# Optimization experiments

Measured on AMD Instinct MI355X. Metric: run time of the kernel, lower is better.

## Reference

```python
import jax, jax.numpy as jnp
import numpy as np

B, CIN, H, W = 16, 128, 56, 56
COUT, KH, KW = 256, 3, 3
STRIDE = (1, 1)
PAD = ((1, 1), (1, 1))


def setup_inputs() -> dict:
    key = jax.random.key(0)
    k1, k2, k3 = jax.random.split(key, 3)
    x = jax.random.normal(k1, (B, CIN, H, W), dtype=jnp.float32)
    weight = jax.random.normal(k2, (COUT, CIN, KH, KW), dtype=jnp.float32) * 0.05
    bias = jax.random.normal(k3, (COUT,), dtype=jnp.float32)
    return {"x": x, "weight": weight, "bias": bias}


def reference(x, weight, bias):
    # Conv2d with zero padding, stride 1 -- identical math to the torch
    # unfold+expand+multiply+triple-sum path.
    dn = jax.lax.conv_dimension_numbers(x.shape, weight.shape, ("NCHW", "OIHW", "NCHW"))
    out = jax.lax.conv_general_dilated(x, weight, STRIDE, PAD, dimension_numbers=dn)
    out = out + bias[None, :, None, None]

    # Sparsity of the elementwise product patches * weight.
    # count_nonzero(x_patch * w) over all (b,hw,ww,co,ci,kh,kw) factorizes as
    # sum over windows of conv(1[x!=0], 1[w!=0]) -- same count without
    # materializing the [B,Hw,Ww,Co,Ci,kh,kw] tensor the torch code builds.
    co, ci, kh, kw = weight.shape
    hw, ww = out.shape[2], out.shape[3]
    num_elements = x.shape[0] * hw * ww * co * ci * kh * kw
    nz_map = jax.lax.conv_general_dilated(
        (x != 0).astype(jnp.float32),
        (weight != 0).astype(jnp.float32),
        STRIDE, PAD, dimension_numbers=dn)
    num_nonzero = jnp.sum(nz_map)
    layer_sparsity = (jnp.float32(num_elements) - num_nonzero) / jnp.float32(num_elements)
    return out, layer_sparsity
```

## Files before the change

### kernel.cpp

```cpp
#include <hip/hip_runtime.h>
#include <hip/hip_bf16.h>

typedef __attribute__((ext_vector_type(8))) short bf16x8;
typedef __attribute__((ext_vector_type(8))) unsigned short ushort8;
typedef __attribute__((ext_vector_type(4))) unsigned short ushort4v;
typedef __attribute__((ext_vector_type(4))) float f32x4;
typedef __attribute__((ext_vector_type(4))) unsigned int uint4v;

#define CIN_  128
#define BATCH 16
#define SP_   3136
#define CO_   256
#define NTOT  50176

#define XP_BYTES   13778944
#define WT_BYTES   589824
#define WS_NEEDED  14447104

__device__ __forceinline__ unsigned short f2bf(float f) {
    unsigned int u = __float_as_uint(f);
    u = (u + 0x7fffu + ((u >> 16) & 1u)) >> 16;
    return (unsigned short)u;
}

__device__ __forceinline__ void gl_lds16(const unsigned short* g, unsigned short* l) {
    __builtin_amdgcn_global_load_lds(
        (const __attribute__((address_space(1))) unsigned int*)g,
        (__attribute__((address_space(3))) unsigned int*)l, 16, 0, 0);
}

__global__ __launch_bounds__(256) void k_aux(
    const float* __restrict__ x, const float* __restrict__ w,
    unsigned short* __restrict__ Wt, unsigned short* __restrict__ xp,
    float* __restrict__ Wcnt, float* __restrict__ part)
{
    __shared__ float T[64][65];
    __shared__ float red9[4][9];
    const int blk = blockIdx.x;
    const int tid = threadIdx.x;

    if (blk < 288) {
        int base = (blk * 256 + tid) * 4;
        float4 v = *(const float4*)(w + base);
        #pragma unroll
        for (int j = 0; j < 4; ++j) {
            int e = base + j;
            int co = e / 1152;
            int r  = e - co * 1152;
            int ci = r / 9;
            int koff = r - ci * 9;
            Wt[(koff * 256 + co) * 128 + ci] = f2bf(((const float*)&v)[j]);
        }
    } else if (blk < 576) {
        int lane = tid & 63;
        int j = (blk - 288) * 4 + (tid >> 6);
        float c = 0.f;
        for (int co = lane; co < 256; co += 64)
            c += (w[(size_t)co * 1152 + j] != 0.0f) ? 1.f : 0.f;
        #pragma unroll
        for (int s = 32; s > 0; s >>= 1) c += __shfl_down(c, s, 64);
        if (lane == 0) Wcnt[j] = c;
    } else if (blk < 2624) {
        int bc = blk - 576;
        int ci = bc & 127;
        int b  = bc >> 7;
        const float* xpk = x + (size_t)bc * SP_;
        float cnt[9];
        #pragma unroll
        for (int k = 0; k < 9; ++k) cnt[k] = 0.f;
        for (int e = tid; e < SP_; e += 256) {
            float v = xpk[e];
            if (v != 0.f) {
                int h = e / 56, w_ = e - h * 56;
                float r0 = (h <= 54) ? 1.f : 0.f;
                float r2 = (h >= 1) ? 1.f : 0.f;
                float c0 = (w_ <= 54) ? 1.f : 0.f;
                float c2 = (w_ >= 1) ? 1.f : 0.f;
                cnt[0] += r0 * c0; cnt[1] += r0; cnt[2] += r0 * c2;
                cnt[3] += c0;      cnt[4] += 1.f; cnt[5] += c2;
                cnt[6] += r2 * c0; cnt[7] += r2; cnt[8] += r2 * c2;
            }
        }
        #pragma unroll
        for (int k = 0; k < 9; ++k) {
            #pragma unroll
            for (int s = 32; s > 0; s >>= 1) cnt[k] += __shfl_down(cnt[k], s, 64);
        }
        if ((tid & 63) == 0) {
            #pragma unroll
            for (int k = 0; k < 9; ++k) red9[tid >> 6][k] = cnt[k];
        }
        __syncthreads();
        if (tid < 9) {
            float s = red9[0][tid] + red9[1][tid] + red9[2][tid] + red9[3][tid];
            part[(ci * 9 + tid) * 16 + b] = s;
        }
    } else if (blk < 4192) {
        int i = blk - 2624;
        int sp0 = (i % 49) * 64;
        int rest = i / 49;
        int ci0 = (rest & 1) * 64;
        int b = rest >> 1;
        const float* xb = x + ((size_t)(b * 128 + ci0)) * SP_ + sp0;
        #pragma unroll
        for (int r = 0; r < 16; ++r) {
            const int ci_l = (tid >> 6) * 16 + r;
            const int sp_l = tid & 63;
            T[sp_l][ci_l] = xb[(size_t)ci_l * SP_ + sp_l];
        }
        __syncthreads();
        #pragma unroll
        for (int r = 0; r < 4; ++r) {
            const int sp_l = (tid >> 4) * 4 + r;
            const int cc   = (tid & 15) * 4;
            const int sp = sp0 + sp_l;
            const int oh = sp / 56, ow = sp - oh * 56;
            ushort4v v;
            #pragma unroll
            for (int j = 0; j < 4; ++j) v[j] = f2bf(T[sp_l][cc + j]);
            *(ushort4v*)&xp[(((size_t)b * 58 + oh + 1) * 58 + (ow + 1)) * 128 + ci0 + cc] = v;
        }
    } else {
        int b = blk - 4192;
        if (tid < 228) {
            int oh, ow;
            if (tid < 58)       { oh = 0;            ow = tid; }
            else if (tid < 116) { oh = 57;           ow = tid - 58; }
            else if (tid < 172) { oh = tid - 116 + 1; ow = 0; }
            else                { oh = tid - 172 + 1; ow = 57; }
            unsigned short* p = xp + (((size_t)b * 58 + oh) * 58 + ow) * 128;
            ushort8 z = {};
            #pragma unroll
            for (int j = 0; j < 16; ++j) *(ushort8*)(p + j * 8) = z;
        }
    }
}

__global__ void k_spars(const float* __restrict__ Wcnt, const float* __restrict__ part,
                        float* __restrict__ out_scalar) {
    __shared__ double red[256];
    int t = threadIdx.x;
    double s = 0.0;
    for (int j = t; j < 1152; j += 256) {
        const float4* p4 = (const float4*)(part + (size_t)j * 16);
        float4 a = p4[0], b = p4[1], c = p4[2], d = p4[3];
        float xs = (a.x + a.y + a.z + a.w) + (b.x + b.y + b.z + b.w)
                 + (c.x + c.y + c.z + c.w) + (d.x + d.y + d.z + d.w);
        s += (double)Wcnt[j] * (double)xs;
    }
    red[t] = s; __syncthreads();
    for (int k = 128; k > 0; k >>= 1) {
        if (t < k) red[t] += red[t + k];
        __syncthreads();
    }
    if (t == 0) {
        const double ne = 14797504512.0;
        out_scalar[0] = (float)((ne - red[0]) / ne);
    }
}

__global__ __launch_bounds__(256, 2) void k_convp(
    const unsigned short* __restrict__ xp, const unsigned short* __restrict__ Wt,
    const float* __restrict__ bias, float* __restrict__ out)
{
    __shared__ __attribute__((aligned(16))) unsigned short Albs[4 * 4096];
    __shared__ __attribute__((aligned(16))) unsigned short Blbs[4 * 4096];

    const int tid  = threadIdx.x;
    const int lane = tid & 63;
    const int l15  = lane & 15;
    const int w    = tid >> 6;
    const int wm   = w >> 1;
    const int wn   = w & 1;

    const int flat = blockIdx.x;
    const int wg   = (flat & 7) * 98 + (flat >> 3);
    const int n0   = (wg >> 1) * 128;
    const int co0  = (wg & 1) * 128;

    int xoffA[2], woffB[2];
    #pragma unroll
    for (int j = 0; j < 2; ++j) {
        int g   = j * 256 + tid;
        int row = g >> 2;
        int c   = (g & 3) ^ ((row >> 1) & 3);
        int n   = n0 + row;
        int b   = n / SP_;
        int sp  = n - b * SP_;
        int oh  = sp / 56, ow = sp - oh * 56;
        xoffA[j] = ((b * 58 + oh + 1) * 58 + (ow + 1)) * 128 + c * 8;
        woffB[j] = (co0 + row) * 128 + c * 8;
    }

    auto stage_p = [&](int p) {
        int ko = p >> 2, q = p & 3;
        int kd = ko / 3;
        int xsh = ((kd - 1) * 58 + (ko - kd * 3 - 1)) * 128 + q * 32;
        int wsh = ko * 32768 + q * 32;
        #pragma unroll
        for (int j = 0; j < 2; ++j)
            gl_lds16(xp + xsh + xoffA[j], &Albs[q * 4096 + (j * 256 + tid) * 8]);
        #pragma unroll
        for (int j = 0; j < 2; ++j)
            gl_lds16(Wt + wsh + woffB[j], &Blbs[q * 4096 + (j * 256 + tid) * 8]);
    };

    f32x4 acc[4][4] = {};
    const int cl = lane >> 4;

#define LDA_(SLOT, R) \
    (*(const bf16x8*)&Albs[(SLOT) * 4096 + ((R) + l15) * 32 + \
        ((cl ^ ((((R) + l15) >> 1) & 3)) * 8)])
#define LDB_(SLOT, R) \
    (*(const bf16x8*)&Blbs[(SLOT) * 4096 + ((R) + l15) * 32 + \
        ((cl ^ ((((R) + l15) >> 1) & 3)) * 8)])

    stage_p(0); stage_p(1);
    asm volatile("s_waitcnt vmcnt(4)" ::: "memory");
    __builtin_amdgcn_s_barrier();

    #pragma unroll 1
    for (int p = 0; p < 36; ++p) {
        const int slot = p & 3;

        if (p < 34) {
            stage_p(p + 2);
            asm volatile("s_waitcnt vmcnt(4)" ::: "memory");
        } else if (p == 34) {
            asm volatile("s_waitcnt vmcnt(4)" ::: "memory");
        } else {
            asm volatile("s_waitcnt vmcnt(0)" ::: "memory");
        }
        __builtin_amdgcn_s_barrier();

        bf16x8 b_[4], a_[4];
        #pragma unroll
        for (int nn = 0; nn < 4; ++nn) b_[nn] = LDB_(slot, wn * 64 + nn * 16);
        #pragma unroll
        for (int m = 0; m < 4; ++m)    a_[m] = LDA_(slot, wm * 64 + m * 16);

        __builtin_amdgcn_s_setprio(1);
        #pragma unroll
        for (int m = 0; m < 4; ++m)
            #pragma unroll
            for (int nn = 0; nn < 4; ++nn)
                acc[m][nn] = __builtin_amdgcn_mfma_f32_16x16x32_bf16(
                    a_[m], b_[nn], acc[m][nn], 0, 0, 0);
        __builtin_amdgcn_s_setprio(0);
    }

#undef LDA_
#undef LDB_

    #pragma unroll
    for (int m = 0; m < 4; ++m) {
        int n  = n0 + wm * 64 + m * 16 + (lane >> 4) * 4;
        int b  = n / SP_;
        int sp = n - b * SP_;
        #pragma unroll
        for (int nn = 0; nn < 4; ++nn) {
            int co = co0 + wn * 64 + nn * 16 + l15;
            f32x4 v = acc[m][nn] + bias[co];
            *(f32x4*)&out[((size_t)(b * CO_ + co)) * SP_ + sp] = v;
        }
    }
}

__global__ void k_wt(const float* __restrict__ w, unsigned short* __restrict__ Wt) {
    int e = blockIdx.x * 256 + threadIdx.x;
    float v = w[e];
    int co = e / 1152;
    int r  = e - co * 1152;
    int ci = r / 9;
    int koff = r - ci * 9;
    Wt[(koff * 256 + co) * 128 + ci] = f2bf(v);
}

__global__ void k_wcnt(const float* __restrict__ w, float* __restrict__ Wcnt) {
    int j = blockIdx.x;
    int lane = threadIdx.x;
    float c = 0.f;
    for (int co = lane; co < 256; co += 64)
        c += (w[(size_t)co * 1152 + j] != 0.0f) ? 1.f : 0.f;
    #pragma unroll
    for (int s = 32; s > 0; s >>= 1) c += __shfl_down(c, s, 64);
    if (lane == 0) Wcnt[j] = c;
}

__global__ void k_xcnt(const float* __restrict__ x, float* __restrict__ Xcnt) {
    int blk = blockIdx.x;
    int ci = blk & 127;
    const float* xpk = x + (size_t)blk * SP_;
    int tid = threadIdx.x;
    float cnt[9];
    #pragma unroll
    for (int k = 0; k < 9; ++k) cnt[k] = 0.f;
    for (int e = tid; e < SP_; e += 256) {
        float v = xpk[e];
        if (v != 0.f) {
            int h = e / 56, w_ = e - h * 56;
            float r0 = (h <= 54) ? 1.f : 0.f;
            float r2 = (h >= 1) ? 1.f : 0.f;
            float c0 = (w_ <= 54) ? 1.f : 0.f;
            float c2 = (w_ >= 1) ? 1.f : 0.f;
            cnt[0] += r0 * c0; cnt[1] += r0; cnt[2] += r0 * c2;
            cnt[3] += c0;      cnt[4] += 1.f; cnt[5] += c2;
            cnt[6] += r2 * c0; cnt[7] += r2; cnt[8] += r2 * c2;
        }
    }
    #pragma unroll
    for (int k = 0; k < 9; ++k) {
        #pragma unroll
        for (int s = 32; s > 0; s >>= 1) cnt[k] += __shfl_down(cnt[k], s, 64);
    }
    if ((tid & 63) == 0) {
        #pragma unroll
        for (int k = 0; k < 9; ++k)
            atomicAdd(&Xcnt[ci * 9 + k], cnt[k]);
    }
}

__global__ void k_spars_f(const float* __restrict__ Wcnt, const float* __restrict__ Xcnt,
                          float* __restrict__ out_scalar) {
    __shared__ double red[256];
    int t = threadIdx.x;
    double s = 0.0;
    for (int j = t; j < 1152; j += 256)
        s += (double)Wcnt[j] * (double)Xcnt[j];
    red[t] = s; __syncthreads();
    for (int k = 128; k > 0; k >>= 1) {
        if (t < k) red[t] += red[t + k];
        __syncthreads();
    }
    if (t == 0) {
        const double ne = 14797504512.0;
        out_scalar[0] = (float)((ne - red[0]) / ne);
    }
}

__global__ __launch_bounds__(256) void k_conv(
    const float* __restrict__ x, const unsigned short* __restrict__ Wt,
    const float* __restrict__ bias, float* __restrict__ out)
{
    __shared__ __attribute__((aligned(16))) unsigned short AldsF[64][40];
    __shared__ __attribute__((aligned(16))) unsigned short BldsF[64][40];

    const int tid  = threadIdx.x;
    const int lane = tid & 63;
    const int wid  = tid >> 6;
    const int wm   = wid >> 1, wn = wid & 1;

    const int n0  = blockIdx.x * 64;
    const int b   = blockIdx.x / 49;
    const int sp0 = n0 - b * SP_;
    const int co0 = blockIdx.y * 64;

    const int a_co = tid >> 2;
    const int a_ci = (tid & 3) * 8;
    const int b_n  = tid & 63;
    const int b_k0 = (tid >> 6) * 8;

    const int sp = sp0 + b_n;
    const int oh = sp / 56, ow = sp - oh * 56;

    f32x4 acc[2][2] = {};
    const float* xb_base = x + (size_t)b * CIN_ * SP_;

    for (int koff = 0; koff < 9; ++koff) {
        const int dh = koff / 3 - 1, dw = koff - (koff / 3) * 3 - 1;
        const int ih = oh + dh, iw = ow + dw;
        const bool valid = ((unsigned)ih < 56u) && ((unsigned)iw < 56u);
        const float* xb = xb_base + sp + dh * 56 + dw;
        const unsigned short* wp = Wt + ((size_t)(koff * 256 + co0 + a_co)) * 128 + a_ci;

        for (int ci0 = 0; ci0 < 128; ci0 += 32) {
            uint4v av = *(const uint4v*)(wp + ci0);
            *(uint4v*)&AldsF[a_co][a_ci] = av;
            ushort8 bv;
            #pragma unroll
            for (int j = 0; j < 8; ++j) {
                int ci = ci0 + b_k0 + j;
                float v = 0.f;
                if (valid) v = xb[(size_t)ci * SP_];
                bv[j] = f2bf(v);
            }
            *(ushort8*)&BldsF[b_n][b_k0] = bv;
            __syncthreads();

            const int row = lane & 15;
            const int kq  = (lane >> 4) * 8;
            bf16x8 a0 = *(const bf16x8*)&AldsF[wm * 32 + row][kq];
            bf16x8 a1 = *(const bf16x8*)&AldsF[wm * 32 + 16 + row][kq];
            bf16x8 bb0 = *(const bf16x8*)&BldsF[wn * 32 + row][kq];
            bf16x8 bb1 = *(const bf16x8*)&BldsF[wn * 32 + 16 + row][kq];
            acc[0][0] = __builtin_amdgcn_mfma_f32_16x16x32_bf16(a0, bb0, acc[0][0], 0, 0, 0);
            acc[0][1] = __builtin_amdgcn_mfma_f32_16x16x32_bf16(a0, bb1, acc[0][1], 0, 0, 0);
            acc[1][0] = __builtin_amdgcn_mfma_f32_16x16x32_bf16(a1, bb0, acc[1][0], 0, 0, 0);
            acc[1][1] = __builtin_amdgcn_mfma_f32_16x16x32_bf16(a1, bb1, acc[1][1], 0, 0, 0);
            __syncthreads();
        }
    }

    const int col = lane & 15;
    const int rb  = (lane >> 4) * 4;
    #pragma unroll
    for (int f = 0; f < 2; ++f) {
        #pragma unroll
        for (int g = 0; g < 2; ++g) {
            int spc = sp0 + wn * 32 + g * 16 + col;
            #pragma unroll
            for (int r = 0; r < 4; ++r) {
                int co = co0 + wm * 32 + f * 16 + rb + r;
                out[((size_t)(b * CO_ + co)) * SP_ + spc] = acc[f][g][r] + bias[co];
            }
        }
    }
}

extern "C" void kernel_launch(void* const* d_in, const int* in_sizes, int n_in,
                              void* d_out, int out_size, void* d_ws, size_t ws_size,
                              hipStream_t stream) {
    const float* x    = (const float*)d_in[0];
    const float* w    = (const float*)d_in[1];
    const float* bias = (const float*)d_in[2];
    float* out = (float*)d_out;

    if (ws_size >= (size_t)WS_NEEDED) {
        unsigned short* xp = (unsigned short*)d_ws;
        unsigned short* Wt = (unsigned short*)((char*)d_ws + XP_BYTES);
        float* Wcnt = (float*)((char*)d_ws + XP_BYTES + WT_BYTES);
        float* part = Wcnt + 1152;

        hipLaunchKernelGGL(k_aux,   dim3(4208),   dim3(256), 0, stream,
                           x, w, Wt, xp, Wcnt, part);
        hipLaunchKernelGGL(k_convp, dim3(784),    dim3(256), 0, stream, xp, Wt, bias, out);
        hipLaunchKernelGGL(k_spars, dim3(1),      dim3(256), 0, stream, Wcnt, part,
                           out + 12845056);
    } else {
        unsigned short* Wt = (unsigned short*)d_ws;
        float* Wcnt = (float*)((char*)d_ws + WT_BYTES);
        float* Xcnt = Wcnt + 1152;

        hipMemsetAsync((void*)Xcnt, 0, 1152 * sizeof(float), stream);
        hipLaunchKernelGGL(k_wt,      dim3(1152),    dim3(256), 0, stream, w, Wt);
        hipLaunchKernelGGL(k_wcnt,    dim3(1152),    dim3(64),  0, stream, w, Wcnt);
        hipLaunchKernelGGL(k_xcnt,    dim3(2048),    dim3(256), 0, stream, x, Xcnt);
        hipLaunchKernelGGL(k_conv,    dim3(784, 4),  dim3(256), 0, stream, x, Wt, bias, out);
        hipLaunchKernelGGL(k_spars_f, dim3(1),       dim3(256), 0, stream, Wcnt, Xcnt,
                           out + 12845056);
    }
}
```

Before: 75.24 us.

## Use full-Cout 128x256 tiles with B read from global and fold sparsity reduction into conv

Replaces the 128x128-tile conv with a 512-thread kernel where each block covers all 256 output channels for 128 spatial rows. Only A (input patches) is staged through LDS with double buffering over 64-channel K steps, and B (weights) is loaded straight from global/L2 into registers. The sparsity reduction kernel is merged into an extra block of the conv launch, which removes one kernel launch. In exchange there are only 393 blocks, so each CU gets fewer waves, and register pressure rises from holding the B fragments.

```diff
diff --git a/kernel.cpp b/kernel.cpp
--- a/kernel.cpp
+++ b/kernel.cpp
@@ -136,121 +136,118 @@
     }
 }
 
-__global__ void k_spars(const float* __restrict__ Wcnt, const float* __restrict__ part,
-                        float* __restrict__ out_scalar) {
-    __shared__ double red[256];
-    int t = threadIdx.x;
-    double s = 0.0;
-    for (int j = t; j < 1152; j += 256) {
-        const float4* p4 = (const float4*)(part + (size_t)j * 16);
-        float4 a = p4[0], b = p4[1], c = p4[2], d = p4[3];
-        float xs = (a.x + a.y + a.z + a.w) + (b.x + b.y + b.z + b.w)
-                 + (c.x + c.y + c.z + c.w) + (d.x + d.y + d.z + d.w);
-        s += (double)Wcnt[j] * (double)xs;
-    }
-    red[t] = s; __syncthreads();
-    for (int k = 128; k > 0; k >>= 1) {
-        if (t < k) red[t] += red[t + k];
-        __syncthreads();
-    }
-    if (t == 0) {
-        const double ne = 14797504512.0;
-        out_scalar[0] = (float)((ne - red[0]) / ne);
-    }
-}
-
-__global__ __launch_bounds__(256, 2) void k_convp(
+__global__ __launch_bounds__(512, 4) void k_convg(
     const unsigned short* __restrict__ xp, const unsigned short* __restrict__ Wt,
-    const float* __restrict__ bias, float* __restrict__ out)
+    const float* __restrict__ bias, float* __restrict__ out,
+    const float* __restrict__ Wcnt, const float* __restrict__ part)
 {
-    __shared__ __attribute__((aligned(16))) unsigned short Albs[4 * 4096];
-    __shared__ __attribute__((aligned(16))) unsigned short Blbs[4 * 4096];
+    __shared__ __attribute__((aligned(16))) unsigned short Albs[2 * 8192];
 
     const int tid  = threadIdx.x;
+
+    if (blockIdx.x == 392) {
+        __shared__ double red[512];
+        double s = 0.0;
+        for (int j = tid; j < 1152; j += 512) {
+            const float4* p4 = (const float4*)(part + (size_t)j * 16);
+            float4 a = p4[0], b = p4[1], c = p4[2], d = p4[3];
+            float xs = (a.x + a.y + a.z + a.w) + (b.x + b.y + b.z + b.w)
+                     + (c.x + c.y + c.z + c.w) + (d.x + d.y + d.z + d.w);
+            s += (double)Wcnt[j] * (double)xs;
+        }
+        red[tid] = s; __syncthreads();
+        for (int k = 256; k > 0; k >>= 1) {
+            if (tid < k) red[tid] += red[tid + k];
+            __syncthreads();
+        }
+        if (tid == 0) {
+            const double ne = 14797504512.0;
+            out[12845056] = (float)((ne - red[0]) / ne);
+        }
+        return;
+    }
+
     const int lane = tid & 63;
     const int l15  = lane & 15;
+    const int cl   = lane >> 4;
     const int w    = tid >> 6;
-    const int wm   = w >> 1;
-    const int wn   = w & 1;
-
-    const int flat = blockIdx.x;
-    const int wg   = (flat & 7) * 98 + (flat >> 3);
-    const int n0   = (wg >> 1) * 128;
-    const int co0  = (wg & 1) * 128;
-
-    int xoffA[2], woffB[2];
+    const int wm   = w >> 2;
+    const int wn   = w & 3;
+    const int n0   = blockIdx.x * 128;
+
+    int xoffA[2];
     #pragma unroll
     for (int j = 0; j < 2; ++j) {
-        int g   = j * 256 + tid;
-        int row = g >> 2;
-        int c   = (g & 3) ^ ((row >> 1) & 3);
+        int g   = j * 512 + tid;
+        int row = g >> 3;
+        int c   = (g & 7) ^ (row & 7);
         int n   = n0 + row;
         int b   = n / SP_;
         int sp  = n - b * SP_;
         int oh  = sp / 56, ow = sp - oh * 56;
         xoffA[j] = ((b * 58 + oh + 1) * 58 + (ow + 1)) * 128 + c * 8;
-        woffB[j] = (co0 + row) * 128 + c * 8;
-    }
-
-    auto stage_p = [&](int p) {
-        int ko = p >> 2, q = p & 3;
-        int kd = ko / 3;
-        int xsh = ((kd - 1) * 58 + (ko - kd * 3 - 1)) * 128 + q * 32;
-        int wsh = ko * 32768 + q * 32;
+    }
+
+    auto stageA = [&](int kt) {
+        int koff = kt >> 1;
+        int kd   = koff / 3;
+        int xsh  = ((kd - 1) * 58 + (koff - kd * 3 - 1)) * 128 + (kt & 1) * 64;
+        unsigned short* dst = Albs + (kt & 1) * 8192;
         #pragma unroll
         for (int j = 0; j < 2; ++j)
-            gl_lds16(xp + xsh + xoffA[j], &Albs[q * 4096 + (j * 256 + tid) * 8]);
-        #pragma unroll
-        for (int j = 0; j < 2; ++j)
-            gl_lds16(Wt + wsh + woffB[j], &Blbs[q * 4096 + (j * 256 + tid) * 8]);
+            gl_lds16(xp + xsh + xoffA[j], dst + (j * 512 + tid) * 8);
     };
 
     f32x4 acc[4][4] = {};
-    const int cl = lane >> 4;
-
-#define LDA_(SLOT, R) \
-    (*(const bf16x8*)&Albs[(SLOT) * 4096 + ((R) + l15) * 32 + \
-        ((cl ^ ((((R) + l15) >> 1) & 3)) * 8)])
-#define LDB_(SLOT, R) \
-    (*(const bf16x8*)&Blbs[(SLOT) * 4096 + ((R) + l15) * 32 + \
-        ((cl ^ ((((R) + l15) >> 1) & 3)) * 8)])
-
-    stage_p(0); stage_p(1);
-    asm volatile("s_waitcnt vmcnt(4)" ::: "memory");
-    __builtin_amdgcn_s_barrier();
+
+#define LDA_(BO, S, M)                                                         \
+    (*(const bf16x8*)&Albs[(BO) + (wm * 64 + (M) * 16 + l15) * 64 +            \
+        ((((S) * 4 + cl) ^ ((wm * 64 + (M) * 16 + l15) & 7)) * 8)])
+
+    stageA(0);
 
     #pragma unroll 1
-    for (int p = 0; p < 36; ++p) {
-        const int slot = p & 3;
-
-        if (p < 34) {
-            stage_p(p + 2);
-            asm volatile("s_waitcnt vmcnt(4)" ::: "memory");
-        } else if (p == 34) {
-            asm volatile("s_waitcnt vmcnt(4)" ::: "memory");
+    for (int kt = 0; kt < 18; ++kt) {
+        const int bo   = (kt & 1) * 8192;
+        const int koff = kt >> 1;
+        const int half = kt & 1;
+
+        bf16x8 bfr[2][4];
+        {
+            const unsigned short* wb = Wt + koff * 32768 + half * 64 + cl * 8;
+            #pragma unroll
+            for (int S = 0; S < 2; ++S)
+                #pragma unroll
+                for (int nn = 0; nn < 4; ++nn)
+                    bfr[S][nn] = *(const bf16x8*)(wb + (wn * 64 + nn * 16 + l15) * 128 + S * 32);
+        }
+
+        if (kt < 17) {
+            stageA(kt + 1);
+            asm volatile("s_waitcnt vmcnt(10)" ::: "memory");
         } else {
-            asm volatile("s_waitcnt vmcnt(0)" ::: "memory");
+            asm volatile("s_waitcnt vmcnt(8)" ::: "memory");
         }
         __builtin_amdgcn_s_barrier();
 
-        bf16x8 b_[4], a_[4];
-        #pragma unroll
-        for (int nn = 0; nn < 4; ++nn) b_[nn] = LDB_(slot, wn * 64 + nn * 16);
-        #pragma unroll
-        for (int m = 0; m < 4; ++m)    a_[m] = LDA_(slot, wm * 64 + m * 16);
-
-        __builtin_amdgcn_s_setprio(1);
-        #pragma unroll
-        for (int m = 0; m < 4; ++m)
-            #pragma unroll
-            for (int nn = 0; nn < 4; ++nn)
-                acc[m][nn] = __builtin_amdgcn_mfma_f32_16x16x32_bf16(
-                    a_[m], b_[nn], acc[m][nn], 0, 0, 0);
-        __builtin_amdgcn_s_setprio(0);
+        #pragma unroll
+        for (int S = 0; S < 2; ++S) {
+            bf16x8 a_[4];
+            #pragma unroll
+            for (int m = 0; m < 4; ++m) a_[m] = LDA_(bo, S, m);
+            __builtin_amdgcn_s_setprio(1);
+            #pragma unroll
+            for (int m = 0; m < 4; ++m)
+                #pragma unroll
+                for (int nn = 0; nn < 4; ++nn)
+                    acc[m][nn] = __builtin_amdgcn_mfma_f32_16x16x32_bf16(
+                        a_[m], bfr[S][nn], acc[m][nn], 0, 0, 0);
+            __builtin_amdgcn_s_setprio(0);
+        }
+        __builtin_amdgcn_s_barrier();
     }
 
 #undef LDA_
-#undef LDB_
 
     #pragma unroll
     for (int m = 0; m < 4; ++m) {
@@ -259,7 +256,7 @@
         int sp = n - b * SP_;
         #pragma unroll
         for (int nn = 0; nn < 4; ++nn) {
-            int co = co0 + wn * 64 + nn * 16 + l15;
+            int co = wn * 64 + nn * 16 + l15;
             f32x4 v = acc[m][nn] + bias[co];
             *(f32x4*)&out[((size_t)(b * CO_ + co)) * SP_ + sp] = v;
         }
@@ -433,9 +430,8 @@
 
         hipLaunchKernelGGL(k_aux,   dim3(4208),   dim3(256), 0, stream,
                            x, w, Wt, xp, Wcnt, part);
-        hipLaunchKernelGGL(k_convp, dim3(784),    dim3(256), 0, stream, xp, Wt, bias, out);
-        hipLaunchKernelGGL(k_spars, dim3(1),      dim3(256), 0, stream, Wcnt, part,
-                           out + 12845056);
+        hipLaunchKernelGGL(k_convg, dim3(393),    dim3(512), 0, stream,
+                           xp, Wt, bias, out, Wcnt, part);
     } else {
         unsigned short* Wt = (unsigned short*)d_ws;
         float* Wcnt = (float*)((char*)d_ws + WT_BYTES);
```

New measurement: 116.0 us. 54.2% more time.
